# Performance work log

Hardware: AMD Instinct MI355X
Metric: run time of the kernel (lower is better)

## Reference

```python
import jax, jax.numpy as jnp
import numpy as np

NL, DM, DI, DS, DC, DR, NC = 4, 128, 256, 16, 4, 8, 10
ALPHA = 0.3  # observer_alpha

def layernorm(x, w, b, eps=1e-5):
    m = x.mean(-1, keepdims=True)
    v = ((x - m) ** 2).mean(-1, keepdims=True)
    return (x - m) / jnp.sqrt(v + eps) * w + b

def silu(x):
    return x * jax.nn.sigmoid(x)

def causal_dwconv(x, w, b):
    # x: (B, L, DI); w: (DI, 1, DC); b: (DI,)
    xt = x.transpose(0, 2, 1)  # (B, DI, L)
    y = jax.lax.conv_general_dilated(
        xt, w, window_strides=(1,), padding=[(DC - 1, 0)],
        dimension_numbers=('NCH', 'OIH', 'NCH'), feature_group_count=DI)
    return (y + b[None, :, None]).transpose(0, 2, 1)  # (B, L, DI)

def ssm_scan(delta, Bc, Cc, u, A):
    # delta, u: (B, L, DI); Bc, Cc: (B, L, DS); A: (DI, DS)
    B = delta.shape[0]
    def step(h, inp):
        d_t, b_t, c_t, u_t = inp  # (B,DI),(B,DS),(B,DS),(B,DI)
        dA = jnp.exp(d_t[..., None] * A)              # (B, DI, DS)
        h = dA * h + (d_t * u_t)[..., None] * b_t[:, None, :]
        y = jnp.einsum('bds,bs->bd', h, c_t)
        return h, y
    h0 = jnp.zeros((B, DI, DS), delta.dtype)
    xs = (delta.transpose(1, 0, 2), Bc.transpose(1, 0, 2),
          Cc.transpose(1, 0, 2), u.transpose(1, 0, 2))
    _, ys = jax.lax.scan(step, h0, xs)
    return ys.transpose(1, 0, 2)  # (B, L, DI)

def _forward(x, W_in, b_in, ln_w, ln_b, in_proj_w, conv_w, conv_b, x_proj_w,
             dt_proj_w, dt_proj_b, A_log, Dp, out_proj_w, out_proj_b,
             norm_w, norm_b, cls_w, cls_b):
    B = x.shape[0]
    u = x.transpose(0, 2, 3, 1).reshape(B, -1, 3)   # (B, L, 3)
    h = u @ W_in + b_in                              # (B, L, DM)
    for i in range(NL):
        res = h
        z = layernorm(h, ln_w[i], ln_b[i])
        xz = z @ in_proj_w[i]                        # (B, L, 2*DI)
        xin, gate = jnp.split(xz, 2, axis=-1)
        xc = silu(causal_dwconv(xin, conv_w[i], conv_b[i]))  # (B, L, DI)
        proj = xc @ x_proj_w[i]                      # (B, L, DR + 2*DS)
        dt, Bc, Cc = jnp.split(proj, [DR, DR + DS], axis=-1)
        delta = jax.nn.softplus(dt @ dt_proj_w[i] + dt_proj_b[i])  # (B, L, DI)
        A = -jnp.exp(A_log[i])                       # (DI, DS)
        y = ssm_scan(delta, Bc, Cc, xc, A) + xc * Dp[i]
        # Luenberger-style observer correction: blend predicted SSM output
        y = (1.0 - ALPHA) * y + ALPHA * xc
        y = y * silu(gate)
        h = res + y @ out_proj_w[i] + out_proj_b[i]
    pooled = h.mean(axis=1)                          # (B, DM)
    pooled = layernorm(pooled, norm_w, norm_b)
    return pooled @ cls_w + cls_b                    # (B, NC)

def setup_inputs():
    key = jax.random.key(0)
    ks = jax.random.split(key, 8)
    def nrm(k, shape, std=0.02):
        return jax.random.normal(k, shape, jnp.float32) * std
    return {
        'x': jax.random.normal(ks[0], (32, 3, 32, 32), jnp.float32),
        'W_in': nrm(ks[1], (3, DM)), 'b_in': jnp.zeros((DM,), jnp.float32),
        'ln_w': jnp.ones((NL, DM), jnp.float32), 'ln_b': jnp.zeros((NL, DM), jnp.float32),
        'in_proj_w': nrm(ks[2], (NL, DM, 2 * DI)),
        'conv_w': nrm(ks[3], (NL, DI, 1, DC), 0.2), 'conv_b': jnp.zeros((NL, DI), jnp.float32),
        'x_proj_w': nrm(ks[4], (NL, DI, DR + 2 * DS)),
        'dt_proj_w': nrm(ks[5], (NL, DR, DI), 0.1),
        'dt_proj_b': jnp.full((NL, DI), -4.6, jnp.float32),
        'A_log': jnp.log(jnp.broadcast_to(jnp.arange(1, DS + 1, dtype=jnp.float32), (NL, DI, DS))),
        'Dp': jnp.ones((NL, DI), jnp.float32),
        'out_proj_w': nrm(ks[6], (NL, DI, DM)), 'out_proj_b': jnp.zeros((NL, DM), jnp.float32),
        'norm_w': jnp.ones((DM,), jnp.float32), 'norm_b': jnp.zeros((DM,), jnp.float32),
        'cls_w': nrm(ks[7], (DM, NC)), 'cls_b': jnp.zeros((NC,), jnp.float32),
    }

def reference(x, W_in, b_in, ln_w, ln_b, in_proj_w, conv_w, conv_b, x_proj_w,
              dt_proj_w, dt_proj_b, A_log, Dp, out_proj_w, out_proj_b,
              norm_w, norm_b, cls_w, cls_b):
    return _forward(x, W_in, b_in, ln_w, ln_b, in_proj_w, conv_w, conv_b,
                    x_proj_w, dt_proj_w, dt_proj_b, A_log, Dp, out_proj_w,
                    out_proj_b, norm_w, norm_b, cls_w, cls_b)
```

## Files before the change

kernel.cpp:

```cpp
#include <hip/hip_runtime.h>
#include <math.h>

#define B_  32
#define L_  1024
#define T_  (B_ * L_)
#define DM_ 128
#define DI_ 256
#define DS_ 16
#define DC_ 4
#define DR_ 8
#define NC_ 10
#define CHUNK_ 64
#define NCH_  (L_ / CHUNK_)
#define PSTR_ 288

typedef __bf16 bf16x8 __attribute__((ext_vector_type(8)));
typedef __bf16 bf16x4 __attribute__((ext_vector_type(4)));
typedef __bf16 bf16x2 __attribute__((ext_vector_type(2)));
typedef float f32x4 __attribute__((ext_vector_type(4)));
typedef unsigned short u16x8 __attribute__((ext_vector_type(8)));

__device__ __forceinline__ float sigmoidf_(float x) { return 1.0f / (1.0f + __expf(-x)); }
__device__ __forceinline__ float siluf_(float x)    { return x * sigmoidf_(x); }
__device__ __forceinline__ float softplusf_(float x) {
    return (x > 15.0f) ? x : __logf(1.0f + __expf(x));
}
__device__ __forceinline__ float fexp2_(float x) { return __builtin_amdgcn_exp2f(x); }

__device__ __forceinline__ void gload_lds16(const __bf16* g, __bf16* l) {
    __builtin_amdgcn_global_load_lds(
        (const __attribute__((address_space(1))) void*)g,
        (__attribute__((address_space(3))) void*)l, 16, 0, 0);
}

template<int R>
__device__ __forceinline__ void stage_async(const __bf16* __restrict__ src,
        __bf16* lds, int k0, int stride, int wid, int lane) {
    constexpr int NI = R / 32;
#pragma unroll
    for (int j = 0; j < NI; ++j) {
        int s0 = (wid * NI + j) * 64;
        int s = s0 + lane;
        int row = s >> 3, sw = s & 7;
        int slot = sw ^ (row & 7);
        gload_lds16(src + (size_t)row * stride + k0 + slot * 8, lds + (size_t)s0 * 8);
    }
}

__global__ __launch_bounds__(128) void k_embed(const float* __restrict__ x,
        const float* __restrict__ Win, const float* __restrict__ bin,
        float* __restrict__ h) {
    int t = blockIdx.x;
    int b = t >> 10, l = t & 1023;
    int m = threadIdx.x;
    const float* xb = x + (size_t)b * 3 * 1024 + l;
    float acc = bin[m];
    acc = fmaf(xb[0],    Win[m],        acc);
    acc = fmaf(xb[1024], Win[128 + m],  acc);
    acc = fmaf(xb[2048], Win[256 + m],  acc);
    h[(size_t)t * 128 + m] = acc;
}

__global__ __launch_bounds__(256) void k_prep_w(const float* __restrict__ ipw,
        const float* __restrict__ opw, __bf16* __restrict__ wt1,
        __bf16* __restrict__ wt2) {
    int i = blockIdx.x * 256 + threadIdx.x;
    {
        int lay = i >> 16, rem = i & 65535, n = rem >> 7, k = rem & 127;
        wt1[i] = (__bf16)ipw[lay * 65536 + k * 512 + n];
    }
    if (i < 4 * 128 * 256) {
        int lay = i >> 15, rem = i & 32767, n = rem >> 8, k = rem & 255;
        wt2[i] = (__bf16)opw[lay * 32768 + k * 128 + n];
    }
}

__global__ __launch_bounds__(256) void k_prep_wcat(const float* __restrict__ xpw,
        const float* __restrict__ dtw, __bf16* __restrict__ wcat) {
    int blk = blockIdx.x;
    int lay = blk / 384, n = blk % 384;
    int k = threadIdx.x;
    float v;
    if (n < 256) {
        float acc = 0.0f;
#pragma unroll
        for (int r = 0; r < 8; ++r)
            acc = fmaf(xpw[lay * 10240 + k * 40 + r], dtw[lay * 2048 + r * 256 + n], acc);
        v = acc;
    } else if (n < 288) {
        v = xpw[lay * 10240 + k * 40 + (n - 248)];
    } else {
        v = 0.0f;
    }
    wcat[(size_t)blk * 256 + k] = (__bf16)v;
}

__global__ __launch_bounds__(256) void k_ln(const float* __restrict__ h,
        const float* __restrict__ w, const float* __restrict__ b,
        __bf16* __restrict__ z) {
    int wid = threadIdx.x >> 6, lane = threadIdx.x & 63;
    int t = blockIdx.x * 4 + wid;
    const float* hr = h + (size_t)t * 128;
    float2 v = *(const float2*)(hr + lane * 2);
    float s = v.x + v.y, sq = v.x * v.x + v.y * v.y;
#pragma unroll
    for (int off = 1; off < 64; off <<= 1) {
        s += __shfl_xor(s, off);
        sq += __shfl_xor(sq, off);
    }
    float mean = s * (1.0f / 128.0f);
    float var = sq * (1.0f / 128.0f) - mean * mean;
    float rstd = rsqrtf(var + 1e-5f);
    float2 wv = *(const float2*)(w + lane * 2);
    float2 bv = *(const float2*)(b + lane * 2);
    bf16x2 o;
    o.x = (__bf16)((v.x - mean) * rstd * wv.x + bv.x);
    o.y = (__bf16)((v.y - mean) * rstd * wv.y + bv.y);
    *(bf16x2*)(z + (size_t)t * 128 + lane * 2) = o;
}

template<int BM, int K, int N, int MODE, bool GATE>
__global__ __launch_bounds__(256) void k_gemm_mfma(
        const __bf16* __restrict__ A, const __bf16* __restrict__ G,
        const __bf16* __restrict__ Wt, const float* __restrict__ bias,
        float* __restrict__ Cf, __bf16* __restrict__ Cb) {
    static_assert(!GATE || BM == 32, "GATE staging assumes BM=32");
    __shared__ __bf16 As[BM * 64];
    __shared__ __bf16 Bs[128 * 64];
    int tid = threadIdx.x;
    int bm = blockIdx.x, bn = blockIdx.y;
    int lane = tid & 63, wid = tid >> 6;
    int lr = lane & 15, lg = lane >> 4;
    constexpr int MF = BM / 16;

    f32x4 acc[MF][2] = {};
    const __bf16* Asrc = A + (size_t)(bm * BM) * K;
    const __bf16* Bsrc = Wt + (size_t)(bn * 128) * K;

    for (int k0 = 0; k0 < K; k0 += 64) {
        if (GATE) {
            int row = tid >> 3, slot = tid & 7;
            int m = bm * BM + row;
            bf16x8 yv = *(const bf16x8*)(A + (size_t)m * K + k0 + slot * 8);
            bf16x8 gv = *(const bf16x8*)(G + (size_t)m * 512 + 256 + k0 + slot * 8);
            bf16x8 v;
#pragma unroll
            for (int j = 0; j < 8; ++j)
                v[j] = (__bf16)((float)yv[j] * siluf_((float)gv[j]));
            *(bf16x8*)(As + row * 64 + ((slot ^ (row & 7)) * 8)) = v;
        } else {
            stage_async<BM>(Asrc, As, k0, K, wid, lane);
        }
        stage_async<128>(Bsrc, Bs, k0, K, wid, lane);
        __syncthreads();
#pragma unroll
        for (int ks = 0; ks < 2; ++ks) {
            int slotbase = ks * 4 + lg;
            bf16x8 af[MF], bfr[2];
#pragma unroll
            for (int m = 0; m < MF; ++m) {
                int row = m * 16 + lr;
                af[m] = *(const bf16x8*)(As + row * 64 + ((slotbase ^ (row & 7)) * 8));
            }
#pragma unroll
            for (int n = 0; n < 2; ++n) {
                int rn = wid * 32 + n * 16 + lr;
                bfr[n] = *(const bf16x8*)(Bs + rn * 64 + ((slotbase ^ (rn & 7)) * 8));
            }
#pragma unroll
            for (int m = 0; m < MF; ++m)
#pragma unroll
                for (int n = 0; n < 2; ++n)
                    acc[m][n] = __builtin_amdgcn_mfma_f32_16x16x32_bf16(
                        af[m], bfr[n], acc[m][n], 0, 0, 0);
        }
        __syncthreads();
    }
#pragma unroll
    for (int m = 0; m < MF; ++m) {
#pragma unroll
        for (int n = 0; n < 2; ++n) {
            int col = bn * 128 + wid * 32 + n * 16 + lr;
            float bv = (MODE == 2) ? bias[col] : 0.0f;
            float dtbv = (MODE == 1 && col < 256) ? bias[col] : 0.0f;
#pragma unroll
            for (int rg = 0; rg < 4; ++rg) {
                int row = bm * BM + m * 16 + lg * 4 + rg;
                float v = acc[m][n][rg];
                if (MODE == 0) {
                    Cb[(size_t)row * N + col] = (__bf16)v;
                } else if (MODE == 1) {
                    if (col < 256)
                        Cb[(size_t)row * PSTR_ + col] = (__bf16)softplusf_(v + dtbv);
                    else if (col < 288)
                        Cb[(size_t)row * PSTR_ + col] = (__bf16)v;
                } else {
                    float* cp = Cf + (size_t)row * N + col;
                    *cp = *cp + v + bv;
                }
            }
        }
    }
}

__global__ __launch_bounds__(256) void k_conv(const __bf16* __restrict__ xzb,
        const float* __restrict__ cw, const float* __restrict__ cb,
        __bf16* __restrict__ xcb) {
    int t = blockIdx.x * 4 + (threadIdx.x >> 6);
    int d0 = (threadIdx.x & 63) * 4;
    int l = t & 1023;
    const __bf16* xp = xzb + (size_t)t * 512 + d0;
    float4 wv[4];
#pragma unroll
    for (int j = 0; j < 4; ++j) wv[j] = *(const float4*)(cw + (d0 + j) * 4);
    float acc[4] = {cb[d0], cb[d0 + 1], cb[d0 + 2], cb[d0 + 3]};
#pragma unroll
    for (int k = 0; k < 4; ++k) {
        int back = 3 - k;
        if (l >= back) {
            bf16x4 v = *(const bf16x4*)(xp - back * 512);
#pragma unroll
            for (int j = 0; j < 4; ++j)
                acc[j] = fmaf((float)v[j], ((const float*)&wv[j])[k], acc[j]);
        }
    }
    bf16x4 o;
#pragma unroll
    for (int j = 0; j < 4; ++j) o[j] = (__bf16)siluf_(acc[j]);
    *(bf16x4*)(xcb + (size_t)t * 256 + d0) = o;
}

template<bool FINAL>
__global__ __launch_bounds__(128) void k_scan_chunk(
        const __bf16* __restrict__ projall, const __bf16* __restrict__ xcb,
        const float* __restrict__ Alog, const float* __restrict__ Dp,
        float* __restrict__ P, float* __restrict__ S,
        __bf16* __restrict__ yb) {
    __shared__ unsigned du_lds[CHUNK_ * 128];
    __shared__ float bc[CHUNK_ * 32];
    int b = blockIdx.z, c = blockIdx.y, dg = blockIdx.x;
    int tid = threadIdx.x;
    int d = dg * 128 + tid;

    const __bf16* projC = projall + ((size_t)b * 1024 + c * CHUNK_) * PSTR_;
    const __bf16* xcC   = xcb + ((size_t)b * 1024 + c * CHUNK_) * 256 + dg * 128;

#pragma unroll
    for (int r = 0; r < 8; ++r) {
        int item = r * 128 + tid;
        int t = item >> 4, o8 = (item & 15) * 8;
        u16x8 dv = *(const u16x8*)(projC + (size_t)t * PSTR_ + dg * 128 + o8);
        u16x8 xv = *(const u16x8*)(xcC + (size_t)t * 256 + o8);
        uint4 w0, w1;
        w0.x = dv[0] | ((unsigned)xv[0] << 16); w0.y = dv[1] | ((unsigned)xv[1] << 16);
        w0.z = dv[2] | ((unsigned)xv[2] << 16); w0.w = dv[3] | ((unsigned)xv[3] << 16);
        w1.x = dv[4] | ((unsigned)xv[4] << 16); w1.y = dv[5] | ((unsigned)xv[5] << 16);
        w1.z = dv[6] | ((unsigned)xv[6] << 16); w1.w = dv[7] | ((unsigned)xv[7] << 16);
        *(uint4*)(du_lds + t * 128 + o8)     = w0;
        *(uint4*)(du_lds + t * 128 + o8 + 4) = w1;
    }
#pragma unroll
    for (int r = 0; r < 2; ++r) {
        int item = r * 128 + tid;
        int t = item >> 2, g8 = (item & 3) * 8;
        bf16x8 v = *(const bf16x8*)(projC + (size_t)t * PSTR_ + 256 + g8);
        float4 f0 = {(float)v[0], (float)v[1], (float)v[2], (float)v[3]};
        float4 f1 = {(float)v[4], (float)v[5], (float)v[6], (float)v[7]};
        *(float4*)(bc + t * 32 + g8)     = f0;
        *(float4*)(bc + t * 32 + g8 + 4) = f1;
    }

    float aa[16], hs[16];
#pragma unroll
    for (int jj = 0; jj < 4; ++jj) {
        float4 av = *(const float4*)(Alog + (size_t)d * 16 + jj * 4);
        aa[jj * 4 + 0] = -__expf(av.x) * 1.44269504088896f;
        aa[jj * 4 + 1] = -__expf(av.y) * 1.44269504088896f;
        aa[jj * 4 + 2] = -__expf(av.z) * 1.44269504088896f;
        aa[jj * 4 + 3] = -__expf(av.w) * 1.44269504088896f;
    }
    float Dpd = Dp[d];
    size_t psIdx = ((size_t)(b * NCH_ + c)) * 4096 + (size_t)d * 16;
    if (FINAL) {
#pragma unroll
        for (int jj = 0; jj < 4; ++jj) {
            float4 h0 = *(const float4*)(P + psIdx + jj * 4);
            hs[jj * 4 + 0] = h0.x; hs[jj * 4 + 1] = h0.y;
            hs[jj * 4 + 2] = h0.z; hs[jj * 4 + 3] = h0.w;
        }
    } else {
#pragma unroll
        for (int j = 0; j < 16; ++j) hs[j] = 0.0f;
    }
    float cumd = 0.0f;
    __bf16* yC = yb + ((size_t)b * 1024 + c * CHUNK_) * 256 + dg * 128 + tid;

    __syncthreads();
#pragma unroll 2
    for (int tt = 0; tt < CHUNK_; ++tt) {
        unsigned duv = du_lds[tt * 128 + tid];
        float delta_t = __uint_as_float(duv << 16);
        float u = __uint_as_float(duv & 0xffff0000u);
        float du = delta_t * u;
        const float* bcr = bc + tt * 32;
        if (!FINAL) cumd += delta_t;
        float ys = 0.0f;
#pragma unroll
        for (int jj = 0; jj < 4; ++jj) {
            float4 Bv = *(const float4*)(bcr + jj * 4);
            float4 Cv;
            if (FINAL) Cv = *(const float4*)(bcr + 16 + jj * 4);
#pragma unroll
            for (int j = 0; j < 4; ++j) {
                int s = jj * 4 + j;
                float dA = fexp2_(delta_t * aa[s]);
                hs[s] = fmaf(dA, hs[s], du * ((const float*)&Bv)[j]);
                if (FINAL) ys = fmaf(hs[s], ((const float*)&Cv)[j], ys);
            }
        }
        if (FINAL) {
            float yv = fmaf(u, Dpd, ys);
            yv = fmaf(0.7f, yv, 0.3f * u);
            yC[(size_t)tt * 256] = (__bf16)yv;
        }
    }
    if (!FINAL) {
#pragma unroll
        for (int jj = 0; jj < 4; ++jj) {
            float4 pv, sv;
            pv.x = fexp2_(aa[jj * 4 + 0] * cumd);
            pv.y = fexp2_(aa[jj * 4 + 1] * cumd);
            pv.z = fexp2_(aa[jj * 4 + 2] * cumd);
            pv.w = fexp2_(aa[jj * 4 + 3] * cumd);
            sv.x = hs[jj * 4 + 0]; sv.y = hs[jj * 4 + 1];
            sv.z = hs[jj * 4 + 2]; sv.w = hs[jj * 4 + 3];
            *(float4*)(P + psIdx + jj * 4) = pv;
            *(float4*)(S + psIdx + jj * 4) = sv;
        }
    }
}

__global__ __launch_bounds__(256) void k_scan_combine(float* __restrict__ P,
        const float* __restrict__ S) {
    int idx = blockIdx.x * 256 + threadIdx.x;
    int b = idx >> 12, rem = idx & 4095;
    float h = 0.0f;
#pragma unroll
    for (int c = 0; c < NCH_; ++c) {
        size_t base = ((size_t)(b * NCH_ + c)) * 4096 + rem;
        float p = P[base];
        float s = S[base];
        P[base] = h;
        h = fmaf(p, h, s);
    }
}

__global__ __launch_bounds__(128) void k_pool(const float* __restrict__ h,
        float* __restrict__ partial) {
    int b = blockIdx.x, lc = blockIdx.y;
    int m = threadIdx.x;
    const float* hb = h + (size_t)b * 131072 + (size_t)lc * 128 * 128 + m;
    float acc = 0.0f;
#pragma unroll 8
    for (int l = 0; l < 128; ++l) acc += hb[(size_t)l * 128];
    partial[((size_t)b * 8 + lc) * 128 + m] = acc;
}

__global__ __launch_bounds__(128) void k_head(const float* __restrict__ partial,
        const float* __restrict__ nw, const float* __restrict__ nb,
        const float* __restrict__ cw, const float* __restrict__ cb,
        float* __restrict__ out) {
    __shared__ float zs[128];
    __shared__ float red[128];
    int b = blockIdx.x, m = threadIdx.x;
    float v = 0.0f;
#pragma unroll
    for (int lc = 0; lc < 8; ++lc) v += partial[((size_t)b * 8 + lc) * 128 + m];
    v *= (1.0f / 1024.0f);
    red[m] = v;
    __syncthreads();
    for (int off = 64; off; off >>= 1) {
        if (m < off) red[m] += red[m + off];
        __syncthreads();
    }
    float mean = red[0] * (1.0f / 128.0f);
    __syncthreads();
    float dv = v - mean;
    red[m] = dv * dv;
    __syncthreads();
    for (int off = 64; off; off >>= 1) {
        if (m < off) red[m] += red[m + off];
        __syncthreads();
    }
    float rstd = rsqrtf(red[0] * (1.0f / 128.0f) + 1e-5f);
    zs[m] = dv * rstd * nw[m] + nb[m];
    __syncthreads();
    if (m < NC_) {
        float acc = cb[m];
#pragma unroll 8
        for (int k = 0; k < 128; ++k) acc = fmaf(zs[k], cw[k * 10 + m], acc);
        out[b * 10 + m] = acc;
    }
}

extern "C" void kernel_launch(void* const* d_in, const int* in_sizes, int n_in,
                              void* d_out, int out_size, void* d_ws, size_t ws_size,
                              hipStream_t stream) {
    const float* x    = (const float*)d_in[0];
    const float* Win  = (const float*)d_in[1];
    const float* bin  = (const float*)d_in[2];
    const float* lnw  = (const float*)d_in[3];
    const float* lnb  = (const float*)d_in[4];
    const float* ipw  = (const float*)d_in[5];
    const float* cw   = (const float*)d_in[6];
    const float* cb   = (const float*)d_in[7];
    const float* xpw  = (const float*)d_in[8];
    const float* dtw  = (const float*)d_in[9];
    const float* dtb  = (const float*)d_in[10];
    const float* Alog = (const float*)d_in[11];
    const float* Dp   = (const float*)d_in[12];
    const float* opw  = (const float*)d_in[13];
    const float* opb  = (const float*)d_in[14];
    const float* nw   = (const float*)d_in[15];
    const float* nb   = (const float*)d_in[16];
    const float* clw  = (const float*)d_in[17];
    const float* clb  = (const float*)d_in[18];

    float* ws = (float*)d_ws;
    float*  h       = ws;
    float*  P       = ws + 4194304;
    float*  Sb      = ws + 6291456;
    __bf16* zb      = (__bf16*)P;
    __bf16* xzb     = (__bf16*)(ws + 8388608);
    __bf16* xcb     = (__bf16*)(ws + 16777216);
    __bf16* projall = (__bf16*)(ws + 20971520);
    __bf16* yb      = (__bf16*)(ws + 25690112);
    float*  partial = ws + 29884416;
    __bf16* wt1     = (__bf16*)(ws + 29917184);
    __bf16* wt2     = (__bf16*)(ws + 30048256);
    __bf16* wcat    = (__bf16*)(ws + 30113792);

    k_prep_w<<<1024, 256, 0, stream>>>(ipw, opw, wt1, wt2);
    k_prep_wcat<<<4 * 384, 256, 0, stream>>>(xpw, dtw, wcat);
    k_embed<<<T_, 128, 0, stream>>>(x, Win, bin, h);
    for (int lay = 0; lay < 4; ++lay) {
        k_ln<<<T_ / 4, 256, 0, stream>>>(h, lnw + lay * 128, lnb + lay * 128, zb);
        k_gemm_mfma<64, 128, 512, 0, false><<<dim3(T_ / 64, 4), 256, 0, stream>>>(
            zb, nullptr, wt1 + (size_t)lay * 65536, nullptr, nullptr, xzb);
        k_conv<<<T_ / 4, 256, 0, stream>>>(xzb, cw + lay * 1024, cb + lay * 256, xcb);
        k_gemm_mfma<64, 256, 384, 1, false><<<dim3(T_ / 64, 3), 256, 0, stream>>>(
            xcb, nullptr, wcat + (size_t)lay * 98304, dtb + lay * 256, nullptr, projall);
        k_scan_chunk<false><<<dim3(2, NCH_, B_), 128, 0, stream>>>(projall, xcb,
            Alog + lay * 4096, Dp + lay * 256, P, Sb, yb);
        k_scan_combine<<<B_ * 4096 / 256, 256, 0, stream>>>(P, Sb);
        k_scan_chunk<true><<<dim3(2, NCH_, B_), 128, 0, stream>>>(projall, xcb,
            Alog + lay * 4096, Dp + lay * 256, P, Sb, yb);
        k_gemm_mfma<32, 256, 128, 2, true><<<dim3(T_ / 32, 1), 256, 0, stream>>>(
            yb, xzb, wt2 + (size_t)lay * 32768, opb + lay * 128, h, nullptr);
    }
    k_pool<<<dim3(32, 8), 128, 0, stream>>>(h, partial);
    k_head<<<32, 128, 0, stream>>>(partial, nw, nb, clw, clb, (float*)d_out);
}
```

Measured before the change: 639.6 us.

## Fuse next-layer LayerNorm into out-proj GEMM, fold scan combine into final pass

```diff
diff --git a/kernel.cpp b/kernel.cpp
--- a/kernel.cpp
+++ b/kernel.cpp
@@ -61,38 +61,38 @@
     h[(size_t)t * 128 + m] = acc;
 }
 
-__global__ __launch_bounds__(256) void k_prep_w(const float* __restrict__ ipw,
-        const float* __restrict__ opw, __bf16* __restrict__ wt1,
-        __bf16* __restrict__ wt2) {
-    int i = blockIdx.x * 256 + threadIdx.x;
-    {
+__global__ __launch_bounds__(256) void k_prep(const float* __restrict__ ipw,
+        const float* __restrict__ opw, const float* __restrict__ xpw,
+        const float* __restrict__ dtw, __bf16* __restrict__ wt1,
+        __bf16* __restrict__ wt2, __bf16* __restrict__ wcat) {
+    int blk = blockIdx.x;
+    int tid = threadIdx.x;
+    int i = blk * 256 + tid;
+    if (i < 262144) {
         int lay = i >> 16, rem = i & 65535, n = rem >> 7, k = rem & 127;
         wt1[i] = (__bf16)ipw[lay * 65536 + k * 512 + n];
     }
-    if (i < 4 * 128 * 256) {
+    if (i < 131072) {
         int lay = i >> 15, rem = i & 32767, n = rem >> 8, k = rem & 255;
         wt2[i] = (__bf16)opw[lay * 32768 + k * 128 + n];
     }
-}
-
-__global__ __launch_bounds__(256) void k_prep_wcat(const float* __restrict__ xpw,
-        const float* __restrict__ dtw, __bf16* __restrict__ wcat) {
-    int blk = blockIdx.x;
-    int lay = blk / 384, n = blk % 384;
-    int k = threadIdx.x;
-    float v;
-    if (n < 256) {
-        float acc = 0.0f;
-#pragma unroll
-        for (int r = 0; r < 8; ++r)
-            acc = fmaf(xpw[lay * 10240 + k * 40 + r], dtw[lay * 2048 + r * 256 + n], acc);
-        v = acc;
-    } else if (n < 288) {
-        v = xpw[lay * 10240 + k * 40 + (n - 248)];
-    } else {
-        v = 0.0f;
-    }
-    wcat[(size_t)blk * 256 + k] = (__bf16)v;
+    {
+        int lay = blk / 384, n = blk % 384;
+        int k = tid;
+        float v;
+        if (n < 256) {
+            float acc = 0.0f;
+#pragma unroll
+            for (int r = 0; r < 8; ++r)
+                acc = fmaf(xpw[lay * 10240 + k * 40 + r], dtw[lay * 2048 + r * 256 + n], acc);
+            v = acc;
+        } else if (n < 288) {
+            v = xpw[lay * 10240 + k * 40 + (n - 248)];
+        } else {
+            v = 0.0f;
+        }
+        wcat[(size_t)blk * 256 + k] = (__bf16)v;
+    }
 }
 
 __global__ __launch_bounds__(256) void k_ln(const float* __restrict__ h,
@@ -119,14 +119,19 @@
     *(bf16x2*)(z + (size_t)t * 128 + lane * 2) = o;
 }
 
-template<int BM, int K, int N, int MODE, bool GATE>
+template<int BM, int K, int N, int MODE, bool GATE, bool WLN>
 __global__ __launch_bounds__(256) void k_gemm_mfma(
         const __bf16* __restrict__ A, const __bf16* __restrict__ G,
         const __bf16* __restrict__ Wt, const float* __restrict__ bias,
-        float* __restrict__ Cf, __bf16* __restrict__ Cb) {
+        float* __restrict__ Cf, __bf16* __restrict__ Cb,
+        const float* __restrict__ lnw, const float* __restrict__ lnb,
+        __bf16* __restrict__ Zb) {
     static_assert(!GATE || BM == 32, "GATE staging assumes BM=32");
+    static_assert(!WLN || (MODE == 2 && BM == 32 && N == 128), "WLN geometry");
     __shared__ __bf16 As[BM * 64];
     __shared__ __bf16 Bs[128 * 64];
+    __shared__ float red_s[WLN ? 4 : 1][WLN ? 32 : 1];
+    __shared__ float red_q[WLN ? 4 : 1][WLN ? 32 : 1];
     int tid = threadIdx.x;
     int bm = blockIdx.x, bn = blockIdx.y;
     int lane = tid & 63, wid = tid >> 6;
@@ -176,6 +181,7 @@
         }
         __syncthreads();
     }
+    float vv[MF][2][4];
 #pragma unroll
     for (int m = 0; m < MF; ++m) {
 #pragma unroll
@@ -196,10 +202,61 @@
                         Cb[(size_t)row * PSTR_ + col] = (__bf16)v;
                 } else {
                     float* cp = Cf + (size_t)row * N + col;
-                    *cp = *cp + v + bv;
+                    v += *cp + bv;
+                    *cp = v;
+                    vv[m][n][rg] = v;
                 }
             }
         }
+    }
+    if (WLN) {
+        float ps[MF][4], pq[MF][4];
+#pragma unroll
+        for (int m = 0; m < MF; ++m)
+#pragma unroll
+            for (int rg = 0; rg < 4; ++rg) {
+                float a = vv[m][0][rg], bv2 = vv[m][1][rg];
+                ps[m][rg] = a + bv2;
+                pq[m][rg] = a * a + bv2 * bv2;
+            }
+#pragma unroll
+        for (int off = 1; off < 16; off <<= 1) {
+#pragma unroll
+            for (int m = 0; m < MF; ++m)
+#pragma unroll
+                for (int rg = 0; rg < 4; ++rg) {
+                    ps[m][rg] += __shfl_xor(ps[m][rg], off);
+                    pq[m][rg] += __shfl_xor(pq[m][rg], off);
+                }
+        }
+        if (lr == 0) {
+#pragma unroll
+            for (int m = 0; m < MF; ++m)
+#pragma unroll
+                for (int rg = 0; rg < 4; ++rg) {
+                    int rl = m * 16 + lg * 4 + rg;
+                    red_s[wid][rl] = ps[m][rg];
+                    red_q[wid][rl] = pq[m][rg];
+                }
+        }
+        __syncthreads();
+#pragma unroll
+        for (int m = 0; m < MF; ++m)
+#pragma unroll
+            for (int rg = 0; rg < 4; ++rg) {
+                int rl = m * 16 + lg * 4 + rg;
+                float s = red_s[0][rl] + red_s[1][rl] + red_s[2][rl] + red_s[3][rl];
+                float q = red_q[0][rl] + red_q[1][rl] + red_q[2][rl] + red_q[3][rl];
+                float mean = s * (1.0f / 128.0f);
+                float var = q * (1.0f / 128.0f) - mean * mean;
+                float rstd = rsqrtf(var + 1e-5f);
+#pragma unroll
+                for (int n = 0; n < 2; ++n) {
+                    int col = wid * 32 + n * 16 + lr;
+                    float z = (vv[m][n][rg] - mean) * rstd * lnw[col] + lnb[col];
+                    Zb[(size_t)(bm * BM + rl) * 128 + col] = (__bf16)z;
+                }
+            }
     }
 }
 
@@ -281,16 +338,21 @@
     }
     float Dpd = Dp[d];
     size_t psIdx = ((size_t)(b * NCH_ + c)) * 4096 + (size_t)d * 16;
+#pragma unroll
+    for (int j = 0; j < 16; ++j) hs[j] = 0.0f;
     if (FINAL) {
-#pragma unroll
-        for (int jj = 0; jj < 4; ++jj) {
-            float4 h0 = *(const float4*)(P + psIdx + jj * 4);
-            hs[jj * 4 + 0] = h0.x; hs[jj * 4 + 1] = h0.y;
-            hs[jj * 4 + 2] = h0.z; hs[jj * 4 + 3] = h0.w;
-        }
-    } else {
-#pragma unroll
-        for (int j = 0; j < 16; ++j) hs[j] = 0.0f;
+        for (int cc = 0; cc < c; ++cc) {
+            size_t base = ((size_t)(b * NCH_ + cc)) * 4096 + (size_t)d * 16;
+#pragma unroll
+            for (int jj = 0; jj < 4; ++jj) {
+                float4 p = *(const float4*)(P + base + jj * 4);
+                float4 s = *(const float4*)(S + base + jj * 4);
+                hs[jj * 4 + 0] = fmaf(p.x, hs[jj * 4 + 0], s.x);
+                hs[jj * 4 + 1] = fmaf(p.y, hs[jj * 4 + 1], s.y);
+                hs[jj * 4 + 2] = fmaf(p.z, hs[jj * 4 + 2], s.z);
+                hs[jj * 4 + 3] = fmaf(p.w, hs[jj * 4 + 3], s.w);
+            }
+        }
     }
     float cumd = 0.0f;
     __bf16* yC = yb + ((size_t)b * 1024 + c * CHUNK_) * 256 + dg * 128 + tid;
@@ -337,21 +399,6 @@
             *(float4*)(P + psIdx + jj * 4) = pv;
             *(float4*)(S + psIdx + jj * 4) = sv;
         }
-    }
-}
-
-__global__ __launch_bounds__(256) void k_scan_combine(float* __restrict__ P,
-        const float* __restrict__ S) {
-    int idx = blockIdx.x * 256 + threadIdx.x;
-    int b = idx >> 12, rem = idx & 4095;
-    float h = 0.0f;
-#pragma unroll
-    for (int c = 0; c < NCH_; ++c) {
-        size_t base = ((size_t)(b * NCH_ + c)) * 4096 + rem;
-        float p = P[base];
-        float s = S[base];
-        P[base] = h;
-        h = fmaf(p, h, s);
     }
 }
 
@@ -440,23 +487,30 @@
     __bf16* wt2     = (__bf16*)(ws + 30048256);
     __bf16* wcat    = (__bf16*)(ws + 30113792);
 
-    k_prep_w<<<1024, 256, 0, stream>>>(ipw, opw, wt1, wt2);
-    k_prep_wcat<<<4 * 384, 256, 0, stream>>>(xpw, dtw, wcat);
+    k_prep<<<1536, 256, 0, stream>>>(ipw, opw, xpw, dtw, wt1, wt2, wcat);
     k_embed<<<T_, 128, 0, stream>>>(x, Win, bin, h);
+    k_ln<<<T_ / 4, 256, 0, stream>>>(h, lnw, lnb, zb);
     for (int lay = 0; lay < 4; ++lay) {
-        k_ln<<<T_ / 4, 256, 0, stream>>>(h, lnw + lay * 128, lnb + lay * 128, zb);
-        k_gemm_mfma<64, 128, 512, 0, false><<<dim3(T_ / 64, 4), 256, 0, stream>>>(
-            zb, nullptr, wt1 + (size_t)lay * 65536, nullptr, nullptr, xzb);
+        k_gemm_mfma<64, 128, 512, 0, false, false><<<dim3(T_ / 64, 4), 256, 0, stream>>>(
+            zb, nullptr, wt1 + (size_t)lay * 65536, nullptr, nullptr, xzb,
+            nullptr, nullptr, nullptr);
         k_conv<<<T_ / 4, 256, 0, stream>>>(xzb, cw + lay * 1024, cb + lay * 256, xcb);
-        k_gemm_mfma<64, 256, 384, 1, false><<<dim3(T_ / 64, 3), 256, 0, stream>>>(
-            xcb, nullptr, wcat + (size_t)lay * 98304, dtb + lay * 256, nullptr, projall);
+        k_gemm_mfma<64, 256, 384, 1, false, false><<<dim3(T_ / 64, 3), 256, 0, stream>>>(
+            xcb, nullptr, wcat + (size_t)lay * 98304, dtb + lay * 256, nullptr, projall,
+            nullptr, nullptr, nullptr);
         k_scan_chunk<false><<<dim3(2, NCH_, B_), 128, 0, stream>>>(projall, xcb,
             Alog + lay * 4096, Dp + lay * 256, P, Sb, yb);
-        k_scan_combine<<<B_ * 4096 / 256, 256, 0, stream>>>(P, Sb);
         k_scan_chunk<true><<<dim3(2, NCH_, B_), 128, 0, stream>>>(projall, xcb,
             Alog + lay * 4096, Dp + lay * 256, P, Sb, yb);
-        k_gemm_mfma<32, 256, 128, 2, true><<<dim3(T_ / 32, 1), 256, 0, stream>>>(
-            yb, xzb, wt2 + (size_t)lay * 32768, opb + lay * 128, h, nullptr);
+        if (lay < 3) {
+            k_gemm_mfma<32, 256, 128, 2, true, true><<<dim3(T_ / 32, 1), 256, 0, stream>>>(
+                yb, xzb, wt2 + (size_t)lay * 32768, opb + lay * 128, h, nullptr,
+                lnw + (lay + 1) * 128, lnb + (lay + 1) * 128, zb);
+        } else {
+            k_gemm_mfma<32, 256, 128, 2, true, false><<<dim3(T_ / 32, 1), 256, 0, stream>>>(
+                yb, xzb, wt2 + (size_t)lay * 32768, opb + lay * 128, h, nullptr,
+                nullptr, nullptr, nullptr);
+        }
     }
     k_pool<<<dim3(32, 8), 128, 0, stream>>>(h, partial);
     k_head<<<32, 128, 0, stream>>>(partial, nw, nb, clw, clb, (float*)d_out);
```

Result: no change. 642.7 us (+0.5%).
